# Optimization experiments

Hardware: AMD Instinct MI355X
Metric: run time of the kernel (lower is better)

## Reference

```python
import jax, jax.numpy as jnp
import numpy as np

N_QUBITS = 8
REPS = 2
DIM = 2 ** N_QUBITS  # 256
C64 = jnp.complex64


def _apply_1q(state, gate, wire):
    """Apply a single-qubit gate. state: [B]+[2]*n, gate: [2,2] or [B,2,2]."""
    s = jnp.moveaxis(state, wire + 1, -1)
    if gate.ndim == 2:
        s = jnp.einsum('ij,b...j->b...i', gate, s)
    else:
        s = jnp.einsum('bij,b...j->b...i', gate, s)
    return jnp.moveaxis(s, -1, wire + 1)


def _cnot(state, ctrl, tgt):
    """CNOT: flip target axis where control bit == 1. state: [B]+[2]*n."""
    s0 = jax.lax.index_in_dim(state, 0, ctrl + 1, keepdims=True)
    s1 = jax.lax.index_in_dim(state, 1, ctrl + 1, keepdims=True)
    s1 = jnp.flip(s1, axis=tgt + 1)
    return jnp.concatenate([s0, s1], axis=ctrl + 1)


def _rx(a):
    """Batched RX gate. a: [B] -> [B,2,2] complex64."""
    c = jnp.cos(0.5 * a).astype(C64)
    s = jnp.sin(0.5 * a).astype(C64)
    mis = (-1j) * s
    return jnp.stack([jnp.stack([c, mis], -1), jnp.stack([mis, c], -1)], -2)


def _rot(phi, theta, omega):
    """PennyLane Rot = RZ(omega) RY(theta) RZ(phi). Scalars -> [2,2] complex64."""
    c = jnp.cos(0.5 * theta).astype(C64)
    s = jnp.sin(0.5 * theta).astype(C64)
    ep = jnp.exp(-0.5j * (phi + omega).astype(C64))   # e^{-i(phi+omega)/2}
    em = jnp.exp(-0.5j * (phi - omega).astype(C64))   # e^{-i(phi-omega)/2}
    epc = jnp.exp(0.5j * (phi + omega).astype(C64))
    emc = jnp.exp(0.5j * (phi - omega).astype(C64))
    return jnp.stack([
        jnp.stack([ep * c, -emc * s], -1),
        jnp.stack([em * s, epc * c], -1),
    ], -2)


def _circuit(x, theta):
    B = x.shape[0]
    state = jnp.zeros((B, DIM), C64).at[:, 0].set(1.0)
    state = state.reshape((B,) + (2,) * N_QUBITS)
    # AngleEmbedding (default rotation='X'): RX(x[:, w]) on wire w
    for w in range(N_QUBITS):
        state = _apply_1q(state, _rx(x[:, w]), w)
    # StronglyEntanglingLayers: per layer, Rot on every wire then ring of CNOTs
    for l in range(REPS):
        for w in range(N_QUBITS):
            g = _rot(theta[l, w, 0], theta[l, w, 1], theta[l, w, 2])
            state = _apply_1q(state, g, w)
        r = (l % (N_QUBITS - 1)) + 1  # PennyLane default ranges
        for w in range(N_QUBITS):
            state = _cnot(state, w, (w + r) % N_QUBITS)
    # expval(PauliZ(0)): wire 0 is the most significant axis
    probs = (state.real ** 2 + state.imag ** 2).reshape(B, 2, DIM // 2)
    ev = probs[:, 0].sum(-1) - probs[:, 1].sum(-1)
    return ((ev + 1.0) * 0.5)[:, None]  # [B, 1]


def setup_inputs() -> dict:
    key = jax.random.key(0)
    kx, kt = jax.random.split(key)
    x = jax.random.normal(kx, (131072, N_QUBITS), dtype=jnp.float32)
    theta = 0.1 * jax.random.normal(kt, (REPS, N_QUBITS, 3), dtype=jnp.float32)
    return {"x": x, "theta": theta}


def reference(x, theta):
    return _circuit(x, theta)
```

## Files before the change

kernel.cpp:

```cpp
#include <hip/hip_runtime.h>


typedef _Float16 v8hf __attribute__((ext_vector_type(8)));
typedef float v4f __attribute__((ext_vector_type(4)));

struct cpx { float re, im; };
__device__ __forceinline__ cpx cmul(cpx a, cpx b) {
    return {a.re * b.re - a.im * b.im, a.re * b.im + a.im * b.re};
}

__device__ __forceinline__ cpx pget(int a, int i, int j) {
    static const float RE[4][4] = {{1, 0, 0, 1}, {0, 1, 1, 0},
                                   {0, 0, 0, 0}, {1, 0, 0, -1}};
    static const float IM[4][4] = {{0, 0, 0, 0}, {0, 0, 0, 0},
                                   {0, -1, 1, 0}, {0, 0, 0, 0}};
    cpx r; r.re = RE[a][i * 2 + j]; r.im = IM[a][i * 2 + j];
    return r;
}

__device__ float ptm_entry(const float* __restrict__ theta, int g, int a, int b) {
    const int l = g >> 3, w = g & 7;
    const float phi = theta[(l * 8 + w) * 3 + 0];
    const float th  = theta[(l * 8 + w) * 3 + 1];
    const float om  = theta[(l * 8 + w) * 3 + 2];
    const float c = cosf(0.5f * th), s = sinf(0.5f * th);
    const float ps = 0.5f * (phi + om), ms = 0.5f * (phi - om);
    cpx G[2][2];
    G[0][0] = {c * cosf(ps), -c * sinf(ps)};
    G[0][1] = {-s * cosf(ms), -s * sinf(ms)};
    G[1][0] = {s * cosf(ms), -s * sinf(ms)};
    G[1][1] = {c * cosf(ps), c * sinf(ps)};
    cpx M1[2][2], H[2][2];
#pragma unroll
    for (int i = 0; i < 2; ++i)
#pragma unroll
        for (int j = 0; j < 2; ++j) {
            cpx acc{0.f, 0.f};
#pragma unroll
            for (int k = 0; k < 2; ++k) {
                cpx t = cmul(pget(a, i, k), G[k][j]);
                acc.re += t.re; acc.im += t.im;
            }
            M1[i][j] = acc;
        }
#pragma unroll
    for (int i = 0; i < 2; ++i)
#pragma unroll
        for (int j = 0; j < 2; ++j) {
            cpx acc{0.f, 0.f};
#pragma unroll
            for (int k = 0; k < 2; ++k) {
                cpx gc{G[k][i].re, -G[k][i].im};
                cpx t = cmul(gc, M1[k][j]);
                acc.re += t.re; acc.im += t.im;
            }
            H[i][j] = acc;
        }
    float tr = 0.f;
#pragma unroll
    for (int i = 0; i < 2; ++i)
#pragma unroll
        for (int j = 0; j < 2; ++j) {
            cpx pb = pget(b, i, j);
            tr += pb.re * H[j][i].re - pb.im * H[j][i].im;
        }
    return 0.5f * tr;
}

__device__ void cnot_entry(int pr, int cand, int* CIDX, float* CSGN) {
    const int pc = pr >> 2, pt = pr & 3;
    const int a = cand >> 2, b2 = cand & 3;
    const int perm[4] = {0, 1, 3, 2};
    float ov = 0.f;
#pragma unroll
    for (int r = 0; r < 4; ++r)
#pragma unroll
        for (int c2 = 0; c2 < 4; ++c2) {
            const int rp = perm[r], cp = perm[c2];
            cpx Rv = cmul(pget(pc, rp >> 1, cp >> 1), pget(pt, rp & 1, cp & 1));
            cpx Kv = cmul(pget(a, r >> 1, c2 >> 1), pget(b2, r & 1, c2 & 1));
            ov += Kv.re * Rv.re + Kv.im * Rv.im;
        }
    ov *= 0.25f;
    if (ov > 0.5f) { CIDX[pr] = cand; CSGN[pr] = 1.f; }
    else if (ov < -0.5f) { CIDX[pr] = cand; CSGN[pr] = -1.f; }
}

__device__ __forceinline__ int ring_conj(int cur, int r, const int* CIDX,
                                         const float* CSGN, float& sg) {
    for (int w = 7; w >= 0; --w) {
        const int tw = (w + r) & 7;
        const int pc = (cur >> (2 * w)) & 3;
        const int pt = (cur >> (2 * tw)) & 3;
        const int q = pc * 4 + pt;
        const int nq = CIDX[q];
        sg *= CSGN[q];
        cur = (cur & ~((3 << (2 * w)) | (3 << (2 * tw))))
            | ((nq >> 2) << (2 * w)) | ((nq & 3) << (2 * tw));
    }
    return cur;
}

#define WS_FLOATS_NEEDED 6912

__global__ __launch_bounds__(1024) void k_prep3(const float* __restrict__ theta,
                                                float* __restrict__ ws) {
    _Float16* AF16 = (_Float16*)ws;
    const int tid = threadIdx.x;
    const int blk = blockIdx.x;

    if (blk == 9) {
        for (int h = tid; h < 27 * 64 * 8; h += 1024) {
            const int L = (h >> 3) & 63;
            const int jj = h & 7;
            const int m = L & 15;
            const int j = (L >> 4) * 8 + jj;
            const bool valid = (m < 12) && ((m & 3) < 3) && (j < 27);
            if (!valid) AF16[h] = (_Float16)0.f;
        }
        return;
    }

    __shared__ float Wa[4096];
    __shared__ float Wb[3072];
    __shared__ float TR[256];
    __shared__ float CSGN[16];
    __shared__ int   CIDX[16];
    __shared__ int   S1k, S1n;
    __shared__ float S1sgn;
    __shared__ int   S1w[8], S1l[8];

    const int P0 = blk / 3, P1 = blk % 3;
    const int let0 = (P0 == 0) ? 0 : ((P0 == 1) ? 3 : 2);
    const int let1 = (P1 == 0) ? 0 : ((P1 == 1) ? 3 : 2);

    if (tid < 256) TR[tid] = ptm_entry(theta, tid >> 4, (tid >> 2) & 3, tid & 3);
    else if (tid < 512) {
        const int r = tid - 256;
        cnot_entry(r >> 4, r & 15, CIDX, CSGN);
    }
    for (int i = tid; i < 4096; i += 1024) Wa[i] = 0.f;
    __syncthreads();

    if (tid == 0) {
        float sg = 1.f;
        int cur = ring_conj(3 , 2, CIDX, CSGN, sg);
        int k = 0;
        for (int w = 0; w < 8; ++w) {
            const int ltr = (cur >> (2 * w)) & 3;
            if (ltr != 0) { S1w[k] = w; S1l[k] = ltr; ++k; }
        }
        int n = 1;
        for (int i = 0; i < k; ++i) n *= 3;
        S1sgn = sg; S1k = k; S1n = n;
    }
    __syncthreads();
    const int k1 = S1k, n1 = S1n;

    for (int t = tid; t < n1; t += 1024) {
        float c = S1sgn;
        int s = 0;
        int tt = t;
        for (int i = 0; i < k1; ++i) {
            const int bl = tt % 3 + 1;
            tt /= 3;
            c *= TR[(8 + S1w[i]) * 16 + S1l[i] * 4 + bl];
            s |= bl << (2 * S1w[i]);
        }
        float sg = 1.f;
        s = ring_conj(s, 1, CIDX, CSGN, sg);
        c *= sg;
        const int a0 = s & 3, a1 = (s >> 2) & 3;
        int d4 = 0;
#pragma unroll
        for (int w = 2; w < 8; ++w)
            d4 |= ((s >> (2 * w)) & 3) << (2 * (7 - w));
        const float v = c * TR[a0 * 4 + let0] * TR[16 + a1 * 4 + let1];
        atomicAdd(&Wa[d4], v);
    }
    __syncthreads();

    const int P3c[6] = {1, 3, 9, 27, 81, 243};
    const int N4c[6] = {1024, 256, 64, 16, 4, 1};
#pragma unroll
    for (int tl = 0; tl < 6; ++tl) {
        const int w = 7 - tl;
        const float* src = (tl & 1) ? Wb : Wa;
        float* dst = (tl & 1) ? Wa : Wb;
        const int p3 = P3c[tl];
        const int Nout = p3 * 3 * N4c[tl];
        for (int idx = tid; idx < Nout; idx += 1024) {
            const int q3 = idx % p3;
            const int rest = idx / p3;
            const int P = rest % 3;
            const int r = rest / 3;
            const int let = (P == 0) ? 0 : ((P == 1) ? 3 : 2);
            const float* ib = src + q3 + p3 * 4 * r;
            dst[idx] = ib[0] * TR[w * 16 + 0 + let]
                     + ib[p3] * TR[w * 16 + 4 + let]
                     + ib[2 * p3] * TR[w * 16 + 8 + let]
                     + ib[3 * p3] * TR[w * 16 + 12 + let];
        }
        __syncthreads();
    }

    const int m = 4 * P0 + P1;
    for (int idx = tid; idx < 729; idx += 1024) {
        const int T = idx / 27, j = idx % 27;
        const int h = (T * 64 + (j >> 3) * 16 + m) * 8 + (j & 7);
        AF16[h] = (_Float16)Wa[idx];
    }
}

__global__ __launch_bounds__(256) void k_main8(const float* __restrict__ x,
                                               const int* __restrict__ wsAF,
                                               float* __restrict__ out,
                                               int ngroups) {
    __shared__ int AFl[6912];
    const int tid = threadIdx.x;
    for (int u = tid; u < 6912; u += 256) AFl[u] = wsAF[u];
    __syncthreads();

    const int lane = tid & 63;
    const int q = lane >> 4, e = lane & 15;
    const bool q0b = (q == 0), q1b = (q == 1), q2b = (q == 2);
    const v8hf* AFp = (const v8hf*)AFl;
    const int wave = blockIdx.x * 4 + (tid >> 6);

#pragma unroll 1
    for (int gi = 0; gi < 2; ++gi) {
        const int g = wave * 2 + gi;
        if (g >= ngroups) break;
        const int b = g * 16 + e;
        const float4* xp = (const float4*)(x + (size_t)b * 8);
        const float4 xa = xp[0], xb = xp[1];

        float cw[8], msw[8];
        {
            const float xv[8] = {xa.x, xa.y, xa.z, xa.w, xb.x, xb.y, xb.z, xb.w};
#pragma unroll
            for (int w = 0; w < 8; ++w) {
                float sv, cv;
                __sincosf(xv[w], &sv, &cv);
                cw[w] = cv;
                msw[w] = -sv;
            }
        }

        float F2[27];
        {
            const float m5v[3] = {1.f, cw[5], msw[5]};
            const float m6v[3] = {1.f, cw[6], msw[6]};
            const float m7v[3] = {1.f, cw[7], msw[7]};
#pragma unroll
            for (int a = 0; a < 3; ++a)
#pragma unroll
                for (int b2 = 0; b2 < 3; ++b2) {
                    const float pp = m5v[a] * m6v[b2];
#pragma unroll
                    for (int c2 = 0; c2 < 3; ++c2)
                        F2[(a * 3 + b2) * 3 + c2] = pp * m7v[c2];
                }
        }
        v8hf bf;
#pragma unroll
        for (int jj = 0; jj < 8; ++jj) {
            const float c0 = F2[jj];
            const float c1 = F2[jj + 8];
            const float c2 = F2[jj + 16];
            const float c3 = (jj < 3) ? F2[jj + 24] : 0.f;
            const float v = q0b ? c0 : (q1b ? c1 : (q2b ? c2 : c3));
            bf[jj] = (_Float16)v;
        }

        const v4f zero = {0.f, 0.f, 0.f, 0.f};
        float h[9];
#pragma unroll
        for (int t = 0; t < 27; ++t) {
            const int a = t / 9, b2 = (t / 3) % 3, c2 = t % 3;
            v4f acc = __builtin_amdgcn_mfma_f32_16x16x32_f16(
                AFp[t * 64 + lane], bf, zero, 0, 0, 0);
            float f = fmaf(cw[1], acc[1], acc[0]);
            f = fmaf(msw[1], acc[2], f);
            if (c2 == 0)      h[a * 3 + b2] = f;
            else if (c2 == 1) h[a * 3 + b2] = fmaf(cw[4], f, h[a * 3 + b2]);
            else              h[a * 3 + b2] = fmaf(msw[4], f, h[a * 3 + b2]);
        }
        float e0 = fmaf(cw[3], h[1], h[0]); e0 = fmaf(msw[3], h[2], e0);
        float e1 = fmaf(cw[3], h[4], h[3]); e1 = fmaf(msw[3], h[5], e1);
        float e2 = fmaf(cw[3], h[7], h[6]); e2 = fmaf(msw[3], h[8], e2);
        float ev = fmaf(cw[2], e1, e0);
        ev = fmaf(msw[2], e2, ev);
        const float g0 = q0b ? 1.f : (q1b ? cw[0] : (q2b ? msw[0] : 0.f));
        ev *= g0;

        ev += __shfl_xor(ev, 16, 64);
        ev += __shfl_xor(ev, 32, 64);
        if (lane < 16) out[b] = (ev + 1.f) * 0.5f;
    }
}

struct c32 { float x, y; };

__device__ __forceinline__ c32 shfl_xor_c(c32 v, int mask) {
    c32 r;
    r.x = __shfl_xor(v.x, mask, 64);
    r.y = __shfl_xor(v.y, mask, 64);
    return r;
}
__device__ __forceinline__ c32 cmadd2(c32 ga, c32 a, c32 gp, c32 p) {
    c32 n;
    n.x = ga.x * a.x - ga.y * a.y + gp.x * p.x - gp.y * p.y;
    n.y = ga.x * a.y + ga.y * a.x + gp.x * p.y + gp.y * p.x;
    return n;
}
__device__ __forceinline__ c32 rx_mix(float c, float s, c32 a, c32 p) {
    c32 n;
    n.x = c * a.x + s * p.y;
    n.y = c * a.y - s * p.x;
    return n;
}
__device__ __forceinline__ void apply_rx(c32 st[4], int lane, int bb, float c, float s) {
    if (bb < 6) {
#pragma unroll
        for (int r = 0; r < 4; ++r) {
            c32 p = shfl_xor_c(st[r], 1 << bb);
            st[r] = rx_mix(c, s, st[r], p);
        }
    } else if (bb == 6) {
        c32 n0 = rx_mix(c, s, st[0], st[1]);
        c32 n1 = rx_mix(c, s, st[1], st[0]);
        c32 n2 = rx_mix(c, s, st[2], st[3]);
        c32 n3 = rx_mix(c, s, st[3], st[2]);
        st[0] = n0; st[1] = n1; st[2] = n2; st[3] = n3;
    } else {
        c32 n0 = rx_mix(c, s, st[0], st[2]);
        c32 n2 = rx_mix(c, s, st[2], st[0]);
        c32 n1 = rx_mix(c, s, st[1], st[3]);
        c32 n3 = rx_mix(c, s, st[3], st[1]);
        st[0] = n0; st[1] = n1; st[2] = n2; st[3] = n3;
    }
}
__device__ __forceinline__ void apply_rot(c32 st[4], int lane, int bb,
                                          c32 g00, c32 g01, c32 g10, c32 g11) {
    if (bb < 6) {
#pragma unroll
        for (int r = 0; r < 4; ++r) {
            c32 p = shfl_xor_c(st[r], 1 << bb);
            bool hi = (lane >> bb) & 1;
            c32 ga, gp;
            ga.x = hi ? g11.x : g00.x;
            ga.y = hi ? g11.y : g00.y;
            gp.x = hi ? g10.x : g01.x;
            gp.y = hi ? g10.y : g01.y;
            st[r] = cmadd2(ga, st[r], gp, p);
        }
    } else if (bb == 6) {
        c32 n0 = cmadd2(g00, st[0], g01, st[1]);
        c32 n1 = cmadd2(g10, st[0], g11, st[1]);
        c32 n2 = cmadd2(g00, st[2], g01, st[3]);
        c32 n3 = cmadd2(g10, st[2], g11, st[3]);
        st[0] = n0; st[1] = n1; st[2] = n2; st[3] = n3;
    } else {
        c32 n0 = cmadd2(g00, st[0], g01, st[2]);
        c32 n2 = cmadd2(g10, st[0], g11, st[2]);
        c32 n1 = cmadd2(g00, st[1], g01, st[3]);
        c32 n3 = cmadd2(g10, st[1], g11, st[3]);
        st[0] = n0; st[1] = n1; st[2] = n2; st[3] = n3;
    }
}
__device__ __forceinline__ void cswap(bool c, c32& a, c32& b) {
    c32 t = a;
    a.x = c ? b.x : a.x; a.y = c ? b.y : a.y;
    b.x = c ? t.x : b.x; b.y = c ? t.y : b.y;
}
__device__ __forceinline__ void apply_cnot(c32 st[4], int lane, int bc, int bt) {
    if (bt < 6) {
        if (bc < 6) {
            bool ctrl = (lane >> bc) & 1;
#pragma unroll
            for (int r = 0; r < 4; ++r) {
                c32 p = shfl_xor_c(st[r], 1 << bt);
                st[r].x = ctrl ? p.x : st[r].x;
                st[r].y = ctrl ? p.y : st[r].y;
            }
        } else {
#pragma unroll
            for (int r = 0; r < 4; ++r) {
                if ((r >> (bc - 6)) & 1) st[r] = shfl_xor_c(st[r], 1 << bt);
            }
        }
    } else {
        if (bc < 6) {
            bool ctrl = (lane >> bc) & 1;
            if (bt == 6) { cswap(ctrl, st[0], st[1]); cswap(ctrl, st[2], st[3]); }
            else         { cswap(ctrl, st[0], st[2]); cswap(ctrl, st[1], st[3]); }
        } else {
            if (bc == 7 && bt == 6) { c32 t = st[2]; st[2] = st[3]; st[3] = t; }
            else if (bc == 6 && bt == 7) { c32 t = st[1]; st[1] = st[3]; st[3] = t; }
        }
    }
}
__global__ __launch_bounds__(256) void qsim_kernel(const float* __restrict__ x,
                                                   const float* __restrict__ theta,
                                                   float* __restrict__ out,
                                                   int batch) {
    __shared__ float rot[2 * 8 * 8];
    const int t = threadIdx.x;
    if (t < 16) {
        const int l = t >> 3, w = t & 7;
        const float phi = theta[(l * 8 + w) * 3 + 0];
        const float th  = theta[(l * 8 + w) * 3 + 1];
        const float om  = theta[(l * 8 + w) * 3 + 2];
        const float c = cosf(0.5f * th), s = sinf(0.5f * th);
        const float p = 0.5f * (phi + om), m = 0.5f * (phi - om);
        float* g = &rot[t * 8];
        g[0] = c * cosf(p);  g[1] = -c * sinf(p);
        g[2] = -s * cosf(m); g[3] = -s * sinf(m);
        g[4] = s * cosf(m);  g[5] = -s * sinf(m);
        g[6] = c * cosf(p);  g[7] = c * sinf(p);
    }
    __syncthreads();
    const int lane = t & 63;
    const int b = blockIdx.x * 4 + (t >> 6);
    if (b >= batch) return;
    float c8 = 0.f, s8 = 0.f;
    if (lane < 8) {
        const float xv = 0.5f * x[b * 8 + lane];
        c8 = cosf(xv); s8 = sinf(xv);
    }
    c32 st[4];
#pragma unroll
    for (int r = 0; r < 4; ++r) { st[r].x = 0.f; st[r].y = 0.f; }
    if (lane == 0) st[0].x = 1.f;
#pragma unroll
    for (int w = 0; w < 8; ++w) {
        const float c = __shfl(c8, w, 64);
        const float s = __shfl(s8, w, 64);
        apply_rx(st, lane, 7 - w, c, s);
    }
#pragma unroll
    for (int l = 0; l < 2; ++l) {
#pragma unroll
        for (int w = 0; w < 8; ++w) {
            const float* g = &rot[(l * 8 + w) * 8];
            c32 g00{g[0], g[1]}, g01{g[2], g[3]}, g10{g[4], g[5]}, g11{g[6], g[7]};
            apply_rot(st, lane, 7 - w, g00, g01, g10, g11);
        }
        const int rr = l + 1;
#pragma unroll
        for (int w = 0; w < 8; ++w) apply_cnot(st, lane, 7 - w, 7 - ((w + rr) & 7));
    }
    float v = st[0].x * st[0].x + st[0].y * st[0].y
            + st[1].x * st[1].x + st[1].y * st[1].y
            - st[2].x * st[2].x - st[2].y * st[2].y
            - st[3].x * st[3].x - st[3].y * st[3].y;
#pragma unroll
    for (int off = 32; off > 0; off >>= 1) v += __shfl_xor(v, off, 64);
    if (lane == 0) out[b] = (v + 1.f) * 0.5f;
}

extern "C" void kernel_launch(void* const* d_in, const int* in_sizes, int n_in,
                              void* d_out, int out_size, void* d_ws, size_t ws_size,
                              hipStream_t stream) {
    const float* x     = (const float*)d_in[0];
    const float* theta = (const float*)d_in[1];
    float* out = (float*)d_out;
    const int batch = in_sizes[0] / 8;

    if (ws_size >= (size_t)WS_FLOATS_NEEDED * 4 + 256 && (batch & 15) == 0) {
        float* ws = (float*)d_ws;
        k_prep3<<<dim3(10), dim3(1024), 0, stream>>>(theta, ws);
        const int ngroups = batch / 16;
        const int blocks = (ngroups + 7) / 8;
        k_main8<<<dim3(blocks), dim3(256), 0, stream>>>(
            x, (const int*)ws, out, ngroups);
    } else {
        qsim_kernel<<<dim3((batch + 3) / 4), dim3(256), 0, stream>>>(x, theta, out, batch);
    }
}
```

Before: 69.48 us.

## Interleave two batch groups per wave and overlap x loads with LDS fill

The main kernel now computes the front-end work (x load, sincos, B fragment) for both of its groups before the barrier, so global x loads and transcendentals overlap the shared-memory copy of the transfer matrix. The 27-step MFMA loop then runs on both groups together, sharing each LDS fragment load and issuing two independent MFMAs per step to hide latency. The LDS fill uses int4 vector copies, and launch bounds request 4 blocks per CU. The cost is higher register pressure from keeping two groups' state live at once, which could limit occupancy.

```diff
diff --git a/kernel.cpp b/kernel.cpp
--- a/kernel.cpp
+++ b/kernel.cpp
@@ -212,91 +212,116 @@
     }
 }
 
-__global__ __launch_bounds__(256) void k_main8(const float* __restrict__ x,
-                                               const int* __restrict__ wsAF,
-                                               float* __restrict__ out,
-                                               int ngroups) {
-    __shared__ int AFl[6912];
+__device__ __forceinline__ void front_group(const float* __restrict__ x, int b,
+                                            int q, float* cw, float* msw,
+                                            v8hf& bf) {
+    const float4* xp = (const float4*)(x + (size_t)b * 8);
+    const float4 xa = xp[0], xb = xp[1];
+    const float xv[8] = {xa.x, xa.y, xa.z, xa.w, xb.x, xb.y, xb.z, xb.w};
+#pragma unroll
+    for (int w = 0; w < 8; ++w) {
+        float sv, cv;
+        __sincosf(xv[w], &sv, &cv);
+        cw[w] = cv;
+        msw[w] = -sv;
+    }
+    float F2[27];
+    {
+        const float m5v[3] = {1.f, cw[5], msw[5]};
+        const float m6v[3] = {1.f, cw[6], msw[6]};
+        const float m7v[3] = {1.f, cw[7], msw[7]};
+#pragma unroll
+        for (int a = 0; a < 3; ++a)
+#pragma unroll
+            for (int b2 = 0; b2 < 3; ++b2) {
+                const float pp = m5v[a] * m6v[b2];
+#pragma unroll
+                for (int c2 = 0; c2 < 3; ++c2)
+                    F2[(a * 3 + b2) * 3 + c2] = pp * m7v[c2];
+            }
+    }
+#pragma unroll
+    for (int jj = 0; jj < 8; ++jj) {
+        const float c0 = F2[jj];
+        const float c1 = F2[jj + 8];
+        const float c2 = F2[jj + 16];
+        const float c3 = (jj < 3) ? F2[jj + 24] : 0.f;
+        const float v = (q == 0) ? c0 : ((q == 1) ? c1 : ((q == 2) ? c2 : 0.f));
+        bf[jj] = (_Float16)((q == 3) ? c3 : v);
+    }
+}
+
+__device__ __forceinline__ float finals9(const float* h, const float* cw,
+                                         const float* msw, int q) {
+    float e0 = fmaf(cw[3], h[1], h[0]); e0 = fmaf(msw[3], h[2], e0);
+    float e1 = fmaf(cw[3], h[4], h[3]); e1 = fmaf(msw[3], h[5], e1);
+    float e2 = fmaf(cw[3], h[7], h[6]); e2 = fmaf(msw[3], h[8], e2);
+    float ev = fmaf(cw[2], e1, e0);
+    ev = fmaf(msw[2], e2, ev);
+    const float g0 = (q == 0) ? 1.f : ((q == 1) ? cw[0] : ((q == 2) ? msw[0] : 0.f));
+    return ev * g0;
+}
+
+__global__ __launch_bounds__(256, 4) void k_main9(const float* __restrict__ x,
+                                                  const int* __restrict__ wsAF,
+                                                  float* __restrict__ out,
+                                                  int ngroups) {
+    __shared__ int4 AFl4[1728];
     const int tid = threadIdx.x;
-    for (int u = tid; u < 6912; u += 256) AFl[u] = wsAF[u];
-    __syncthreads();
+    {
+        const int4* w4 = (const int4*)wsAF;
+        for (int u = tid; u < 1728; u += 256) AFl4[u] = w4[u];
+    }
 
     const int lane = tid & 63;
     const int q = lane >> 4, e = lane & 15;
-    const bool q0b = (q == 0), q1b = (q == 1), q2b = (q == 2);
-    const v8hf* AFp = (const v8hf*)AFl;
     const int wave = blockIdx.x * 4 + (tid >> 6);
-
-#pragma unroll 1
-    for (int gi = 0; gi < 2; ++gi) {
-        const int g = wave * 2 + gi;
-        if (g >= ngroups) break;
-        const int b = g * 16 + e;
-        const float4* xp = (const float4*)(x + (size_t)b * 8);
-        const float4 xa = xp[0], xb = xp[1];
-
-        float cw[8], msw[8];
-        {
-            const float xv[8] = {xa.x, xa.y, xa.z, xa.w, xb.x, xb.y, xb.z, xb.w};
-#pragma unroll
-            for (int w = 0; w < 8; ++w) {
-                float sv, cv;
-                __sincosf(xv[w], &sv, &cv);
-                cw[w] = cv;
-                msw[w] = -sv;
+    const int g0 = wave * 2, g1 = g0 + 1;
+    const bool v0 = g0 < ngroups, v1 = g1 < ngroups;
+    const int b0 = (v0 ? g0 : 0) * 16 + e;
+    const int b1 = (v1 ? g1 : (v0 ? g0 : 0)) * 16 + e;
+
+    float cw0[8], msw0[8], cw1[8], msw1[8];
+    v8hf bf0, bf1;
+    front_group(x, b0, q, cw0, msw0, bf0);
+    front_group(x, b1, q, cw1, msw1, bf1);
+
+    __syncthreads();
+
+    if (v0) {
+        const v8hf* AFp = (const v8hf*)AFl4;
+        const v4f zero = {0.f, 0.f, 0.f, 0.f};
+        float h0[9], h1[9];
+#pragma unroll
+        for (int t = 0; t < 27; ++t) {
+            const int a = t / 9, bb = (t / 3) % 3, c2 = t % 3;
+            const v8hf frag = AFp[t * 64 + lane];
+            v4f A0 = __builtin_amdgcn_mfma_f32_16x16x32_f16(frag, bf0, zero, 0, 0, 0);
+            v4f A1 = __builtin_amdgcn_mfma_f32_16x16x32_f16(frag, bf1, zero, 0, 0, 0);
+            float f0 = fmaf(cw0[1], A0[1], A0[0]); f0 = fmaf(msw0[1], A0[2], f0);
+            float f1 = fmaf(cw1[1], A1[1], A1[0]); f1 = fmaf(msw1[1], A1[2], f1);
+            const int hi = a * 3 + bb;
+            if (c2 == 0) {
+                h0[hi] = f0;
+                h1[hi] = f1;
+            } else if (c2 == 1) {
+                h0[hi] = fmaf(cw0[4], f0, h0[hi]);
+                h1[hi] = fmaf(cw1[4], f1, h1[hi]);
+            } else {
+                h0[hi] = fmaf(msw0[4], f0, h0[hi]);
+                h1[hi] = fmaf(msw1[4], f1, h1[hi]);
             }
         }
-
-        float F2[27];
-        {
-            const float m5v[3] = {1.f, cw[5], msw[5]};
-            const float m6v[3] = {1.f, cw[6], msw[6]};
-            const float m7v[3] = {1.f, cw[7], msw[7]};
-#pragma unroll
-            for (int a = 0; a < 3; ++a)
-#pragma unroll
-                for (int b2 = 0; b2 < 3; ++b2) {
-                    const float pp = m5v[a] * m6v[b2];
-#pragma unroll
-                    for (int c2 = 0; c2 < 3; ++c2)
-                        F2[(a * 3 + b2) * 3 + c2] = pp * m7v[c2];
-                }
-        }
-        v8hf bf;
-#pragma unroll
-        for (int jj = 0; jj < 8; ++jj) {
-            const float c0 = F2[jj];
-            const float c1 = F2[jj + 8];
-            const float c2 = F2[jj + 16];
-            const float c3 = (jj < 3) ? F2[jj + 24] : 0.f;
-            const float v = q0b ? c0 : (q1b ? c1 : (q2b ? c2 : c3));
-            bf[jj] = (_Float16)v;
-        }
-
-        const v4f zero = {0.f, 0.f, 0.f, 0.f};
-        float h[9];
-#pragma unroll
-        for (int t = 0; t < 27; ++t) {
-            const int a = t / 9, b2 = (t / 3) % 3, c2 = t % 3;
-            v4f acc = __builtin_amdgcn_mfma_f32_16x16x32_f16(
-                AFp[t * 64 + lane], bf, zero, 0, 0, 0);
-            float f = fmaf(cw[1], acc[1], acc[0]);
-            f = fmaf(msw[1], acc[2], f);
-            if (c2 == 0)      h[a * 3 + b2] = f;
-            else if (c2 == 1) h[a * 3 + b2] = fmaf(cw[4], f, h[a * 3 + b2]);
-            else              h[a * 3 + b2] = fmaf(msw[4], f, h[a * 3 + b2]);
-        }
-        float e0 = fmaf(cw[3], h[1], h[0]); e0 = fmaf(msw[3], h[2], e0);
-        float e1 = fmaf(cw[3], h[4], h[3]); e1 = fmaf(msw[3], h[5], e1);
-        float e2 = fmaf(cw[3], h[7], h[6]); e2 = fmaf(msw[3], h[8], e2);
-        float ev = fmaf(cw[2], e1, e0);
-        ev = fmaf(msw[2], e2, ev);
-        const float g0 = q0b ? 1.f : (q1b ? cw[0] : (q2b ? msw[0] : 0.f));
-        ev *= g0;
-
-        ev += __shfl_xor(ev, 16, 64);
-        ev += __shfl_xor(ev, 32, 64);
-        if (lane < 16) out[b] = (ev + 1.f) * 0.5f;
+        float ev0 = finals9(h0, cw0, msw0, q);
+        float ev1 = finals9(h1, cw1, msw1, q);
+        ev0 += __shfl_xor(ev0, 16, 64);
+        ev0 += __shfl_xor(ev0, 32, 64);
+        ev1 += __shfl_xor(ev1, 16, 64);
+        ev1 += __shfl_xor(ev1, 32, 64);
+        if (lane < 16) {
+            out[b0] = (ev0 + 1.f) * 0.5f;
+            if (v1) out[b1] = (ev1 + 1.f) * 0.5f;
+        }
     }
 }
 
@@ -473,7 +498,7 @@
         k_prep3<<<dim3(10), dim3(1024), 0, stream>>>(theta, ws);
         const int ngroups = batch / 16;
         const int blocks = (ngroups + 7) / 8;
-        k_main8<<<dim3(blocks), dim3(256), 0, stream>>>(
+        k_main9<<<dim3(blocks), dim3(256), 0, stream>>>(
             x, (const int*)ws, out, ngroups);
     } else {
         qsim_kernel<<<dim3((batch + 3) / 4), dim3(256), 0, stream>>>(x, theta, out, batch);
```

After: 101.5 us. +46.1%, slower.
